# Kernel tuning notes

Hardware: AMD Instinct MI355X
Metric: run time of the kernel (lower is better)

The kernel has to match this reference:

```python
import jax, jax.numpy as jnp
import numpy as np

N_NODES = 50000
N_EDGES = 800000
N_GRAPHS = 500
IN_DIM, HID, OUT = 128, 64, 10


def setup_inputs() -> dict:
    key = jax.random.key(0)
    ks = jax.random.split(key, 12)
    x = jax.random.normal(ks[0], (N_NODES, IN_DIM), dtype=jnp.float32)
    edge_index = jax.random.randint(ks[1], (2, N_EDGES), 0, N_NODES, dtype=jnp.int32)
    batch = jnp.sort(jax.random.randint(ks[2], (N_NODES,), 0, N_GRAPHS, dtype=jnp.int32))
    def glorot(k, shape):
        lim = np.sqrt(6.0 / (shape[0] + shape[1]))
        return jax.random.uniform(k, shape, jnp.float32, -lim, lim)
    return {
        "x": x, "edge_index": edge_index, "batch": batch,
        "W1": glorot(ks[3], (IN_DIM, HID)), "b1": jnp.zeros((HID,), jnp.float32),
        "W2": glorot(ks[4], (HID, HID)),    "b2": jnp.zeros((HID,), jnp.float32),
        "W3": glorot(ks[5], (HID, HID)),    "b3": jnp.zeros((HID,), jnp.float32),
        "lin_W1": glorot(ks[6], (HID, HID)), "lin_b1": jnp.zeros((HID,), jnp.float32),
        "lin_W2": glorot(ks[7], (HID, OUT)), "lin_b2": jnp.zeros((OUT,), jnp.float32),
    }


def _gcn_conv(x, src, dst, deg_inv_sqrt, W, b):
    # PyG GCNConv: h = x @ W, then sym-normalized scatter-add over edges (self-loops included in src/dst)
    h = x @ W                                   # [N, out]
    norm = deg_inv_sqrt[src] * deg_inv_sqrt[dst]  # [E+N]
    msgs = h[src] * norm[:, None]               # [E+N, out]  (large gathered intermediate)
    out = jax.ops.segment_sum(msgs, dst, num_segments=N_NODES)
    return out + b


def reference(x, edge_index, batch, W1, b1, W2, b2, W3, b3, lin_W1, lin_b1, lin_W2, lin_b2):
    # add self-loops once; degree (with edge weight 1) computed on target nodes
    loops = jnp.arange(N_NODES, dtype=edge_index.dtype)
    src = jnp.concatenate([edge_index[0], loops])
    dst = jnp.concatenate([edge_index[1], loops])
    deg = jax.ops.segment_sum(jnp.ones_like(dst, dtype=x.dtype), dst, num_segments=N_NODES)
    deg_inv_sqrt = jnp.where(deg > 0, jax.lax.rsqrt(jnp.maximum(deg, 1e-12)), 0.0)

    h = jax.nn.relu(_gcn_conv(x, src, dst, deg_inv_sqrt, W1, b1))
    h = jax.nn.relu(_gcn_conv(h, src, dst, deg_inv_sqrt, W2, b2))
    h = jax.nn.relu(_gcn_conv(h, src, dst, deg_inv_sqrt, W3, b3))

    # global mean pool over graphs
    sums = jax.ops.segment_sum(h, batch, num_segments=N_GRAPHS)
    counts = jax.ops.segment_sum(jnp.ones((h.shape[0],), h.dtype), batch, num_segments=N_GRAPHS)
    pooled = sums / jnp.maximum(counts, 1.0)[:, None]  # [G, HID]

    # MLP head (dropout p=0 / eval -> identity)
    logits = jax.nn.relu(pooled @ lin_W1 + lin_b1) @ lin_W2 + lin_b2
    return (logits, jnp.zeros((), x.dtype))
```

## Files before the change

### kernel.cpp

```cpp
#include <hip/hip_runtime.h>
#include <hip/hip_bf16.h>

#define N_NODES 50000
#define N_EDGES 800000
#define N_GRAPHS 500
#define IN_DIM 128
#define HID 64
#define OUT_DIM 10
#define NB_BUCK ((N_NODES + 63) >> 6)
#define NBLK 256
#define BLDT 1024

__device__ __forceinline__ float bf2f(unsigned short u) {
    return __uint_as_float(((unsigned)u) << 16);
}
__device__ __forceinline__ unsigned short f2bf(float f) {
    unsigned x = __float_as_uint(f);
    x += 0x7fffu + ((x >> 16) & 1u);
    return (unsigned short)(x >> 16);
}
__device__ __forceinline__ void acc8(float a[8], uint4 r) {
    a[0] += __uint_as_float(r.x << 16);
    a[1] += __uint_as_float(r.x & 0xffff0000u);
    a[2] += __uint_as_float(r.y << 16);
    a[3] += __uint_as_float(r.y & 0xffff0000u);
    a[4] += __uint_as_float(r.z << 16);
    a[5] += __uint_as_float(r.z & 0xffff0000u);
    a[6] += __uint_as_float(r.w << 16);
    a[7] += __uint_as_float(r.w & 0xffff0000u);
}

__global__ __launch_bounds__(BLDT) void p1_hist_kernel(const int* __restrict__ dst,
                                                       int* __restrict__ bhist, int e, int epb) {
    __shared__ int h[NB_BUCK];
    int tid = threadIdx.x;
    int blk = blockIdx.x;
    for (int i = tid; i < NB_BUCK; i += BLDT) h[i] = 0;
    __syncthreads();
    int e0 = blk * epb;
    int e1 = e0 + epb;
    if (e1 > e) e1 = e;
    int i = e0 + tid * 4;
    for (; i + 3 < e1; i += BLDT * 4) {
        int4 d4 = *(const int4*)&dst[i];
        atomicAdd(&h[d4.x >> 6], 1);
        atomicAdd(&h[d4.y >> 6], 1);
        atomicAdd(&h[d4.z >> 6], 1);
        atomicAdd(&h[d4.w >> 6], 1);
    }
    for (int k = i; k < e1 && k < i + 4; ++k) atomicAdd(&h[dst[k] >> 6], 1);
    __syncthreads();
    for (int j = tid; j < NB_BUCK; j += BLDT) bhist[blk * NB_BUCK + j] = h[j];
}

__global__ __launch_bounds__(NBLK) void scanA_kernel(int* __restrict__ bhist,
                                                     int* __restrict__ bsum) {
    __shared__ int s[NBLK];
    int b = blockIdx.x;
    int t = threadIdx.x;
    int c = bhist[t * NB_BUCK + b];
    s[t] = c;
    __syncthreads();
    for (int off = 1; off < NBLK; off <<= 1) {
        int x = (t >= off) ? s[t - off] : 0;
        __syncthreads();
        s[t] += x;
        __syncthreads();
    }
    bhist[t * NB_BUCK + b] = s[t] - c;
    if (t == NBLK - 1) bsum[b] = s[t];
}

__global__ __launch_bounds__(BLDT) void p2_place_kernel(
    const int* __restrict__ src, const int* __restrict__ dst,
    const int* __restrict__ bsum, const int* __restrict__ base,
    unsigned* __restrict__ pairs, int* __restrict__ bstart, int e, int epb) {
    __shared__ int h[NB_BUCK];
    __shared__ int sb[NB_BUCK];
    __shared__ int ts[BLDT];
    int tid = threadIdx.x;
    int blk = blockIdx.x;
    int i0 = tid << 2;
    int v0 = 0, v1 = 0, v2 = 0, v3 = 0;
    if (i0 < NB_BUCK) v0 = bsum[i0];
    if (i0 + 1 < NB_BUCK) v1 = bsum[i0 + 1];
    if (i0 + 2 < NB_BUCK) v2 = bsum[i0 + 2];
    if (i0 + 3 < NB_BUCK) v3 = bsum[i0 + 3];
    int tsum = v0 + v1 + v2 + v3;
    ts[tid] = tsum;
    for (int i = tid; i < NB_BUCK; i += BLDT) h[i] = 0;
    __syncthreads();
    for (int off = 1; off < BLDT; off <<= 1) {
        int x = (tid >= off) ? ts[tid - off] : 0;
        __syncthreads();
        ts[tid] += x;
        __syncthreads();
    }
    int excl = ts[tid] - tsum;
    int s0 = excl;
    int s1 = s0 + v0;
    int s2 = s1 + v1;
    int s3 = s2 + v2;
    const int* bb = base + blk * NB_BUCK;
    if (i0 < NB_BUCK) sb[i0] = s0 + bb[i0];
    if (i0 + 1 < NB_BUCK) sb[i0 + 1] = s1 + bb[i0 + 1];
    if (i0 + 2 < NB_BUCK) sb[i0 + 2] = s2 + bb[i0 + 2];
    if (i0 + 3 < NB_BUCK) sb[i0 + 3] = s3 + bb[i0 + 3];
    if (blk == 0) {
        if (i0 < NB_BUCK) bstart[i0] = s0;
        if (i0 + 1 < NB_BUCK) bstart[i0 + 1] = s1;
        if (i0 + 2 < NB_BUCK) bstart[i0 + 2] = s2;
        if (i0 + 3 < NB_BUCK) bstart[i0 + 3] = s3;
        if (tid == 0) bstart[NB_BUCK] = e;
    }
    __syncthreads();
    int e0 = blk * epb;
    int e1 = e0 + epb;
    if (e1 > e) e1 = e;
    int i = e0 + tid * 4;
    for (; i + 3 < e1; i += BLDT * 4) {
        int4 d4 = *(const int4*)&dst[i];
        int4 s4 = *(const int4*)&src[i];
        int b0 = d4.x >> 6, b1 = d4.y >> 6, b2 = d4.z >> 6, b3 = d4.w >> 6;
        int r0 = atomicAdd(&h[b0], 1);
        int r1 = atomicAdd(&h[b1], 1);
        int r2 = atomicAdd(&h[b2], 1);
        int r3 = atomicAdd(&h[b3], 1);
        pairs[sb[b0] + r0] = ((unsigned)(d4.x & 63) << 16) | (unsigned)s4.x;
        pairs[sb[b1] + r1] = ((unsigned)(d4.y & 63) << 16) | (unsigned)s4.y;
        pairs[sb[b2] + r2] = ((unsigned)(d4.z & 63) << 16) | (unsigned)s4.z;
        pairs[sb[b3] + r3] = ((unsigned)(d4.w & 63) << 16) | (unsigned)s4.w;
    }
    for (int k = i; k < e1 && k < i + 4; ++k) {
        int d = dst[k];
        int b = d >> 6;
        int r = atomicAdd(&h[b], 1);
        pairs[sb[b] + r] = ((unsigned)(d & 63) << 16) | (unsigned)src[k];
    }
}

__global__ __launch_bounds__(256) void csr_lin1_kernel(
    const unsigned* __restrict__ pairs, const int* __restrict__ bstart,
    int* __restrict__ rs, float* __restrict__ dinv, int* __restrict__ csr_src,
    const float* __restrict__ A, const float* __restrict__ W,
    unsigned short* __restrict__ C, int n) {
    const int K = IN_DIM;
    __shared__ float As[64][K + 4];
    __shared__ float Ws[K][64];
    __shared__ int lcnt[64];
    __shared__ int lcur[64];
    __shared__ float sdinv[64];
    int b = blockIdx.x;
    int tid = threadIdx.x;
    int beg = bstart[b], end = bstart[b + 1];
    if (tid < 64) lcnt[tid] = 0;
    __syncthreads();
    for (int i = beg + tid; i < end; i += 256) atomicAdd(&lcnt[pairs[i] >> 16], 1);
    __syncthreads();
    if (tid < 64) {
        int c = lcnt[tid];
        int v = c;
#pragma unroll
        for (int off = 1; off < 64; off <<= 1) {
            int t = __shfl_up(v, off);
            if (tid >= off) v += t;
        }
        int excl = v - c;
        int node = b * 64 + tid;
        float dv = rsqrtf((float)(c + 1));
        if (node <= n) {
            rs[node] = beg + excl;
            if (node < n) dinv[node] = dv;
        }
        sdinv[tid] = dv;
        lcur[tid] = beg + excl;
    }
    __syncthreads();
    for (int i = beg + tid; i < end; i += 256) {
        unsigned p = pairs[i];
        int slot = atomicAdd(&lcur[p >> 16], 1);
        csr_src[slot] = (int)(p & 0xffffu);
    }

    int block0 = b * 64;
    int rows = n - block0;
    if (rows > 64) rows = 64;

    const float* Abase = A + (size_t)block0 * K;
    int totalA4 = (rows * K) >> 2;
    for (int i4 = tid; i4 < totalA4; i4 += 256) {
        int i = i4 << 2;
        float4 v = *(const float4*)(Abase + i);
        *(float4*)&As[i / K][i % K] = v;
    }
    {
        const float4* Wv = (const float4*)W;
        float4* Wsv = (float4*)&Ws[0][0];
        for (int i = tid; i < K * 16; i += 256) Wsv[i] = Wv[i];
    }
    __syncthreads();

    int tx = tid & 15;
    int ty = tid >> 4;
    float acc[4][4] = {};
#pragma unroll 2
    for (int k = 0; k < K; k += 4) {
        float4 a[4];
#pragma unroll
        for (int i = 0; i < 4; ++i) a[i] = *(const float4*)&As[ty * 4 + i][k];
        float4 w[4];
#pragma unroll
        for (int kk = 0; kk < 4; ++kk) w[kk] = *(const float4*)&Ws[k + kk][tx * 4];
#pragma unroll
        for (int i = 0; i < 4; ++i) {
            float av[4] = {a[i].x, a[i].y, a[i].z, a[i].w};
#pragma unroll
            for (int kk = 0; kk < 4; ++kk) {
                acc[i][0] += av[kk] * w[kk].x;
                acc[i][1] += av[kk] * w[kk].y;
                acc[i][2] += av[kk] * w[kk].z;
                acc[i][3] += av[kk] * w[kk].w;
            }
        }
    }

#pragma unroll
    for (int i = 0; i < 4; ++i) {
        int r = ty * 4 + i;
        if (r < rows) {
            float s = sdinv[r];
            ushort4 v;
            v.x = f2bf(acc[i][0] * s);
            v.y = f2bf(acc[i][1] * s);
            v.z = f2bf(acc[i][2] * s);
            v.w = f2bf(acc[i][3] * s);
            *(ushort4*)&C[(size_t)(block0 + r) * 64 + tx * 4] = v;
        }
    }
}

__global__ __launch_bounds__(256) void gather_lin_kernel(
    const unsigned short* __restrict__ hs, const int* __restrict__ rs,
    const int* __restrict__ csr_src, const float* __restrict__ dinv,
    const float* __restrict__ bias, const float* __restrict__ W,
    unsigned short* __restrict__ C, int n) {
    const int K = HID;
    __shared__ float As[64][K + 4];
    __shared__ float Ws[K][64];
    int tid = threadIdx.x;
    int b = blockIdx.x;
    int block0 = b * 64;
    int rows = n - block0;
    if (rows > 64) rows = 64;

    {
        const float4* Wv = (const float4*)W;
        float4* Wsv = (float4*)&Ws[0][0];
        for (int i = tid; i < K * 16; i += 256) Wsv[i] = Wv[i];
    }

    int grp = tid >> 3;
    int lg = tid & 7;
    int f8 = lg << 3;
    float4 bb0 = *(const float4*)&bias[f8];
    float4 bb1 = *(const float4*)&bias[f8 + 4];

    for (int r = grp; r < 64; r += 32) {
        int node = block0 + r;
        float a[8] = {0.f, 0.f, 0.f, 0.f, 0.f, 0.f, 0.f, 0.f};
        if (node < n) {
            int beg = rs[node], end = rs[node + 1];
            {
                uint4 u = *(const uint4*)&hs[(size_t)node * 64 + f8];
                acc8(a, u);
            }
            int j = beg;
            for (; j + 3 < end; j += 4) {
                int s0 = csr_src[j];
                int s1 = csr_src[j + 1];
                int s2 = csr_src[j + 2];
                int s3 = csr_src[j + 3];
                uint4 r0 = *(const uint4*)&hs[(size_t)s0 * 64 + f8];
                uint4 r1 = *(const uint4*)&hs[(size_t)s1 * 64 + f8];
                uint4 r2 = *(const uint4*)&hs[(size_t)s2 * 64 + f8];
                uint4 r3 = *(const uint4*)&hs[(size_t)s3 * 64 + f8];
                acc8(a, r0);
                acc8(a, r1);
                acc8(a, r2);
                acc8(a, r3);
            }
            if (j + 1 < end) {
                int s0 = csr_src[j];
                int s1 = csr_src[j + 1];
                uint4 r0 = *(const uint4*)&hs[(size_t)s0 * 64 + f8];
                uint4 r1 = *(const uint4*)&hs[(size_t)s1 * 64 + f8];
                acc8(a, r0);
                acc8(a, r1);
                j += 2;
            }
            if (j < end) {
                int s0 = csr_src[j];
                uint4 r0 = *(const uint4*)&hs[(size_t)s0 * 64 + f8];
                acc8(a, r0);
            }
            float sc = dinv[node];
            a[0] = fmaxf(a[0] * sc + bb0.x, 0.f);
            a[1] = fmaxf(a[1] * sc + bb0.y, 0.f);
            a[2] = fmaxf(a[2] * sc + bb0.z, 0.f);
            a[3] = fmaxf(a[3] * sc + bb0.w, 0.f);
            a[4] = fmaxf(a[4] * sc + bb1.x, 0.f);
            a[5] = fmaxf(a[5] * sc + bb1.y, 0.f);
            a[6] = fmaxf(a[6] * sc + bb1.z, 0.f);
            a[7] = fmaxf(a[7] * sc + bb1.w, 0.f);
        }
        float4 w0 = {a[0], a[1], a[2], a[3]};
        float4 w1 = {a[4], a[5], a[6], a[7]};
        *(float4*)&As[r][f8] = w0;
        *(float4*)&As[r][f8 + 4] = w1;
    }
    __syncthreads();

    int tx = tid & 15;
    int ty = tid >> 4;
    float acc[4][4] = {};
#pragma unroll 2
    for (int k = 0; k < K; k += 4) {
        float4 a[4];
#pragma unroll
        for (int i = 0; i < 4; ++i) a[i] = *(const float4*)&As[ty * 4 + i][k];
        float4 w[4];
#pragma unroll
        for (int kk = 0; kk < 4; ++kk) w[kk] = *(const float4*)&Ws[k + kk][tx * 4];
#pragma unroll
        for (int i = 0; i < 4; ++i) {
            float av[4] = {a[i].x, a[i].y, a[i].z, a[i].w};
#pragma unroll
            for (int kk = 0; kk < 4; ++kk) {
                acc[i][0] += av[kk] * w[kk].x;
                acc[i][1] += av[kk] * w[kk].y;
                acc[i][2] += av[kk] * w[kk].z;
                acc[i][3] += av[kk] * w[kk].w;
            }
        }
    }

#pragma unroll
    for (int i = 0; i < 4; ++i) {
        int r = ty * 4 + i;
        if (r < rows) {
            float s = dinv[block0 + r];
            ushort4 v;
            v.x = f2bf(acc[i][0] * s);
            v.y = f2bf(acc[i][1] * s);
            v.z = f2bf(acc[i][2] * s);
            v.w = f2bf(acc[i][3] * s);
            *(ushort4*)&C[(size_t)(block0 + r) * 64 + tx * 4] = v;
        }
    }
}

__global__ __launch_bounds__(256) void gather_kernel(
    const unsigned short* __restrict__ hs, const int* __restrict__ rs,
    const int* __restrict__ csr_src, const float* __restrict__ dinv,
    const float* __restrict__ bias, unsigned short* __restrict__ outp, int n) {
    int wave = threadIdx.x >> 6;
    int node = blockIdx.x * 4 + wave;
    if (node >= n) return;
    int lane = threadIdx.x & 63;
    int eg = lane >> 3;
    int f8 = (lane & 7) << 3;
    int beg = rs[node], end = rs[node + 1];
    int len = end - beg;
    int q = (len + 7) >> 3;
    int mb = beg + eg * q;
    int me = mb + q;
    if (me > end) me = end;
    float a[8] = {0.f, 0.f, 0.f, 0.f, 0.f, 0.f, 0.f, 0.f};
    if (eg == 0) {
        uint4 r = *(const uint4*)&hs[(size_t)node * 64 + f8];
        acc8(a, r);
    }
    int j = mb;
    for (; j + 3 < me; j += 4) {
        int s0 = csr_src[j];
        int s1 = csr_src[j + 1];
        int s2 = csr_src[j + 2];
        int s3 = csr_src[j + 3];
        uint4 r0 = *(const uint4*)&hs[(size_t)s0 * 64 + f8];
        uint4 r1 = *(const uint4*)&hs[(size_t)s1 * 64 + f8];
        uint4 r2 = *(const uint4*)&hs[(size_t)s2 * 64 + f8];
        uint4 r3 = *(const uint4*)&hs[(size_t)s3 * 64 + f8];
        acc8(a, r0);
        acc8(a, r1);
        acc8(a, r2);
        acc8(a, r3);
    }
    if (j + 1 < me) {
        int s0 = csr_src[j];
        int s1 = csr_src[j + 1];
        uint4 r0 = *(const uint4*)&hs[(size_t)s0 * 64 + f8];
        uint4 r1 = *(const uint4*)&hs[(size_t)s1 * 64 + f8];
        acc8(a, r0);
        acc8(a, r1);
        j += 2;
    }
    if (j < me) {
        int s0 = csr_src[j];
        uint4 r0 = *(const uint4*)&hs[(size_t)s0 * 64 + f8];
        acc8(a, r0);
    }
#pragma unroll
    for (int k = 0; k < 8; ++k) a[k] += __shfl_xor(a[k], 8);
#pragma unroll
    for (int k = 0; k < 8; ++k) a[k] += __shfl_xor(a[k], 16);
#pragma unroll
    for (int k = 0; k < 8; ++k) a[k] += __shfl_xor(a[k], 32);
    if (eg == 0) {
        float s = dinv[node];
        float4 b0 = *(const float4*)&bias[f8];
        float4 b1 = *(const float4*)&bias[f8 + 4];
        float v0 = fmaxf(a[0] * s + b0.x, 0.f);
        float v1 = fmaxf(a[1] * s + b0.y, 0.f);
        float v2 = fmaxf(a[2] * s + b0.z, 0.f);
        float v3 = fmaxf(a[3] * s + b0.w, 0.f);
        float v4 = fmaxf(a[4] * s + b1.x, 0.f);
        float v5 = fmaxf(a[5] * s + b1.y, 0.f);
        float v6 = fmaxf(a[6] * s + b1.z, 0.f);
        float v7 = fmaxf(a[7] * s + b1.w, 0.f);
        uint4 o;
        o.x = (unsigned)f2bf(v0) | ((unsigned)f2bf(v1) << 16);
        o.y = (unsigned)f2bf(v2) | ((unsigned)f2bf(v3) << 16);
        o.z = (unsigned)f2bf(v4) | ((unsigned)f2bf(v5) << 16);
        o.w = (unsigned)f2bf(v6) | ((unsigned)f2bf(v7) << 16);
        *(uint4*)&outp[(size_t)node * 64 + f8] = o;
    }
}

__device__ __forceinline__ int lower_bound_dev(const int* __restrict__ a, int n, int v) {
    int lo = 0, hi = n;
    while (lo < hi) {
        int m = (lo + hi) >> 1;
        if (a[m] < v) lo = m + 1; else hi = m;
    }
    return lo;
}

__global__ __launch_bounds__(1024) void pool_head_kernel(
    const unsigned short* __restrict__ h, const int* __restrict__ batch,
    const float* __restrict__ W1, const float* __restrict__ b1,
    const float* __restrict__ W2, const float* __restrict__ b2,
    float* __restrict__ out, int nNodes, int nGraphs) {
    __shared__ float psum[16][64];
    __shared__ float p[64];
    __shared__ float t64[64];
    int g = blockIdx.x;
    int tid = threadIdx.x;
    int f = tid & 63;
    int q = tid >> 6;
    int lo = lower_bound_dev(batch, nNodes, g);
    int hi = lower_bound_dev(batch, nNodes, g + 1);
    float sum = 0.0f;
    for (int i = lo + q; i < hi; i += 16) sum += bf2f(h[(size_t)i * 64 + f]);
    psum[q][f] = sum;
    __syncthreads();
    if (tid < 64) {
        float s = 0.0f;
#pragma unroll
        for (int w = 0; w < 16; ++w) s += psum[w][f];
        float inv = 1.0f / fmaxf((float)(hi - lo), 1.0f);
        p[f] = s * inv;
        float acc = b1[f];
#pragma unroll
        for (int k = 0; k < 64; ++k) acc += p[k] * W1[k * 64 + f];
        t64[f] = fmaxf(acc, 0.0f);
        if (f < OUT_DIM) {
            float acc2 = b2[f];
#pragma unroll
            for (int k = 0; k < 64; ++k) acc2 += t64[k] * W2[k * OUT_DIM + f];
            out[g * OUT_DIM + f] = acc2;
        }
        if (g == 0 && f == 0) out[nGraphs * OUT_DIM] = 0.0f;
    }
}

extern "C" void kernel_launch(void* const* d_in, const int* in_sizes, int n_in,
                              void* d_out, int out_size, void* d_ws, size_t ws_size,
                              hipStream_t stream) {
    const float* x      = (const float*)d_in[0];
    const int*   eidx   = (const int*)d_in[1];
    const int*   batch  = (const int*)d_in[2];
    const float* W1     = (const float*)d_in[3];
    const float* b1     = (const float*)d_in[4];
    const float* W2     = (const float*)d_in[5];
    const float* b2     = (const float*)d_in[6];
    const float* W3     = (const float*)d_in[7];
    const float* b3     = (const float*)d_in[8];
    const float* lin_W1 = (const float*)d_in[9];
    const float* lin_b1 = (const float*)d_in[10];
    const float* lin_W2 = (const float*)d_in[11];
    const float* lin_b2 = (const float*)d_in[12];
    float* out = (float*)d_out;

    const int E = in_sizes[1] / 2;
    const int N = N_NODES;
    const int NF = N * HID;
    int epb = (E + NBLK - 1) / NBLK;
    epb = (epb + 7) & ~7;

    const int* src = eidx;
    const int* dst = eidx + E;

    unsigned short* buf1 = (unsigned short*)d_ws;
    unsigned short* buf2 = buf1 + NF;
    float* dinv = (float*)(buf2 + NF);
    int* bhist  = (int*)(dinv + N);
    int* bsum   = bhist + NBLK * NB_BUCK;
    int* bstart = bsum + NB_BUCK;
    int* rs     = bstart + NB_BUCK + 1;
    int* csr_src = rs + N + 1;
    unsigned* pairs = (unsigned*)(csr_src + E);

    const int TILES = (N + 63) / 64;
    const int GBLK = (N + 3) / 4;

    p1_hist_kernel<<<NBLK, BLDT, 0, stream>>>(dst, bhist, E, epb);
    scanA_kernel<<<NB_BUCK, NBLK, 0, stream>>>(bhist, bsum);
    p2_place_kernel<<<NBLK, BLDT, 0, stream>>>(src, dst, bsum, bhist, pairs, bstart, E, epb);

    csr_lin1_kernel<<<TILES, 256, 0, stream>>>(pairs, bstart, rs, dinv, csr_src,
                                               x, W1, buf1, N);

    gather_lin_kernel<<<TILES, 256, 0, stream>>>(buf1, rs, csr_src, dinv, b1, W2, buf2, N);

    gather_lin_kernel<<<TILES, 256, 0, stream>>>(buf2, rs, csr_src, dinv, b2, W3, buf1, N);

    gather_kernel<<<GBLK, 256, 0, stream>>>(buf1, rs, csr_src, dinv, b3, buf2, N);

    pool_head_kernel<<<N_GRAPHS, 1024, 0, stream>>>(buf2, batch, lin_W1, lin_b1, lin_W2, lin_b2,
                                                    out, N, N_GRAPHS);
}
```

Measured before the change: 219.2 us.

## Fuse final gather with mean-pool via atomics, shrink gather tiles to 32 rows

The last aggregation layer now accumulates per-graph sums directly with run-length atomics into a global buffer, which is zeroed inside the histogram kernel. This removes the bf16 write and reread of the final node features and the separate pooling pass. The head kernel becomes a small 64-thread kernel that reads those sums. Gather-linear kernels now use 32-row tiles, doubling block count for more parallelism, and the neighbour loop is unrolled by 8 for more loads in flight. Float atomics make the sum order nondeterministic, and the smaller tiles load the weight matrix into shared memory twice as often.

```diff
diff --git a/kernel.cpp b/kernel.cpp
--- a/kernel.cpp
+++ b/kernel.cpp
@@ -30,11 +30,72 @@
     a[7] += __uint_as_float(r.w & 0xffff0000u);
 }
 
+__device__ __forceinline__ void gather_node(const unsigned short* __restrict__ hs,
+                                            const int* __restrict__ csr_src,
+                                            int node, int beg, int end, int f8, float a[8]) {
+    {
+        uint4 u = *(const uint4*)&hs[(size_t)node * 64 + f8];
+        acc8(a, u);
+    }
+    int j = beg;
+    for (; j + 7 < end; j += 8) {
+        int s0 = csr_src[j];
+        int s1 = csr_src[j + 1];
+        int s2 = csr_src[j + 2];
+        int s3 = csr_src[j + 3];
+        int s4 = csr_src[j + 4];
+        int s5 = csr_src[j + 5];
+        int s6 = csr_src[j + 6];
+        int s7 = csr_src[j + 7];
+        uint4 r0 = *(const uint4*)&hs[(size_t)s0 * 64 + f8];
+        uint4 r1 = *(const uint4*)&hs[(size_t)s1 * 64 + f8];
+        uint4 r2 = *(const uint4*)&hs[(size_t)s2 * 64 + f8];
+        uint4 r3 = *(const uint4*)&hs[(size_t)s3 * 64 + f8];
+        uint4 r4 = *(const uint4*)&hs[(size_t)s4 * 64 + f8];
+        uint4 r5 = *(const uint4*)&hs[(size_t)s5 * 64 + f8];
+        uint4 r6 = *(const uint4*)&hs[(size_t)s6 * 64 + f8];
+        uint4 r7 = *(const uint4*)&hs[(size_t)s7 * 64 + f8];
+        acc8(a, r0); acc8(a, r1); acc8(a, r2); acc8(a, r3);
+        acc8(a, r4); acc8(a, r5); acc8(a, r6); acc8(a, r7);
+    }
+    if (j + 3 < end) {
+        int s0 = csr_src[j];
+        int s1 = csr_src[j + 1];
+        int s2 = csr_src[j + 2];
+        int s3 = csr_src[j + 3];
+        uint4 r0 = *(const uint4*)&hs[(size_t)s0 * 64 + f8];
+        uint4 r1 = *(const uint4*)&hs[(size_t)s1 * 64 + f8];
+        uint4 r2 = *(const uint4*)&hs[(size_t)s2 * 64 + f8];
+        uint4 r3 = *(const uint4*)&hs[(size_t)s3 * 64 + f8];
+        acc8(a, r0); acc8(a, r1); acc8(a, r2); acc8(a, r3);
+        j += 4;
+    }
+    if (j + 1 < end) {
+        int s0 = csr_src[j];
+        int s1 = csr_src[j + 1];
+        uint4 r0 = *(const uint4*)&hs[(size_t)s0 * 64 + f8];
+        uint4 r1 = *(const uint4*)&hs[(size_t)s1 * 64 + f8];
+        acc8(a, r0); acc8(a, r1);
+        j += 2;
+    }
+    if (j < end) {
+        int s0 = csr_src[j];
+        uint4 r0 = *(const uint4*)&hs[(size_t)s0 * 64 + f8];
+        acc8(a, r0);
+    }
+}
+
 __global__ __launch_bounds__(BLDT) void p1_hist_kernel(const int* __restrict__ dst,
-                                                       int* __restrict__ bhist, int e, int epb) {
+                                                       int* __restrict__ bhist,
+                                                       float* __restrict__ gsum,
+                                                       int e, int epb) {
     __shared__ int h[NB_BUCK];
     int tid = threadIdx.x;
     int blk = blockIdx.x;
+    {
+        int z = blk * BLDT + tid;
+        if (z < N_GRAPHS * HID) gsum[z] = 0.0f;
+    }
     for (int i = tid; i < NB_BUCK; i += BLDT) h[i] = 0;
     __syncthreads();
     int e0 = blk * epb;
@@ -245,13 +306,12 @@
     const float* __restrict__ bias, const float* __restrict__ W,
     unsigned short* __restrict__ C, int n) {
     const int K = HID;
-    __shared__ float As[64][K + 4];
+    __shared__ float As[32][K + 4];
     __shared__ float Ws[K][64];
     int tid = threadIdx.x;
-    int b = blockIdx.x;
-    int block0 = b * 64;
+    int block0 = blockIdx.x * 32;
     int rows = n - block0;
-    if (rows > 64) rows = 64;
+    if (rows > 32) rows = 32;
 
     {
         const float4* Wv = (const float4*)W;
@@ -265,75 +325,43 @@
     float4 bb0 = *(const float4*)&bias[f8];
     float4 bb1 = *(const float4*)&bias[f8 + 4];
 
-    for (int r = grp; r < 64; r += 32) {
-        int node = block0 + r;
-        float a[8] = {0.f, 0.f, 0.f, 0.f, 0.f, 0.f, 0.f, 0.f};
-        if (node < n) {
-            int beg = rs[node], end = rs[node + 1];
-            {
-                uint4 u = *(const uint4*)&hs[(size_t)node * 64 + f8];
-                acc8(a, u);
-            }
-            int j = beg;
-            for (; j + 3 < end; j += 4) {
-                int s0 = csr_src[j];
-                int s1 = csr_src[j + 1];
-                int s2 = csr_src[j + 2];
-                int s3 = csr_src[j + 3];
-                uint4 r0 = *(const uint4*)&hs[(size_t)s0 * 64 + f8];
-                uint4 r1 = *(const uint4*)&hs[(size_t)s1 * 64 + f8];
-                uint4 r2 = *(const uint4*)&hs[(size_t)s2 * 64 + f8];
-                uint4 r3 = *(const uint4*)&hs[(size_t)s3 * 64 + f8];
-                acc8(a, r0);
-                acc8(a, r1);
-                acc8(a, r2);
-                acc8(a, r3);
-            }
-            if (j + 1 < end) {
-                int s0 = csr_src[j];
-                int s1 = csr_src[j + 1];
-                uint4 r0 = *(const uint4*)&hs[(size_t)s0 * 64 + f8];
-                uint4 r1 = *(const uint4*)&hs[(size_t)s1 * 64 + f8];
-                acc8(a, r0);
-                acc8(a, r1);
-                j += 2;
-            }
-            if (j < end) {
-                int s0 = csr_src[j];
-                uint4 r0 = *(const uint4*)&hs[(size_t)s0 * 64 + f8];
-                acc8(a, r0);
-            }
-            float sc = dinv[node];
-            a[0] = fmaxf(a[0] * sc + bb0.x, 0.f);
-            a[1] = fmaxf(a[1] * sc + bb0.y, 0.f);
-            a[2] = fmaxf(a[2] * sc + bb0.z, 0.f);
-            a[3] = fmaxf(a[3] * sc + bb0.w, 0.f);
-            a[4] = fmaxf(a[4] * sc + bb1.x, 0.f);
-            a[5] = fmaxf(a[5] * sc + bb1.y, 0.f);
-            a[6] = fmaxf(a[6] * sc + bb1.z, 0.f);
-            a[7] = fmaxf(a[7] * sc + bb1.w, 0.f);
-        }
+    int node = block0 + grp;
+    float a[8] = {0.f, 0.f, 0.f, 0.f, 0.f, 0.f, 0.f, 0.f};
+    if (node < n) {
+        int beg = rs[node], end = rs[node + 1];
+        gather_node(hs, csr_src, node, beg, end, f8, a);
+        float sc = dinv[node];
+        a[0] = fmaxf(a[0] * sc + bb0.x, 0.f);
+        a[1] = fmaxf(a[1] * sc + bb0.y, 0.f);
+        a[2] = fmaxf(a[2] * sc + bb0.z, 0.f);
+        a[3] = fmaxf(a[3] * sc + bb0.w, 0.f);
+        a[4] = fmaxf(a[4] * sc + bb1.x, 0.f);
+        a[5] = fmaxf(a[5] * sc + bb1.y, 0.f);
+        a[6] = fmaxf(a[6] * sc + bb1.z, 0.f);
+        a[7] = fmaxf(a[7] * sc + bb1.w, 0.f);
+    }
+    {
         float4 w0 = {a[0], a[1], a[2], a[3]};
         float4 w1 = {a[4], a[5], a[6], a[7]};
-        *(float4*)&As[r][f8] = w0;
-        *(float4*)&As[r][f8 + 4] = w1;
+        *(float4*)&As[grp][f8] = w0;
+        *(float4*)&As[grp][f8 + 4] = w1;
     }
     __syncthreads();
 
     int tx = tid & 15;
     int ty = tid >> 4;
-    float acc[4][4] = {};
+    float acc[2][4] = {};
 #pragma unroll 2
     for (int k = 0; k < K; k += 4) {
-        float4 a[4];
-#pragma unroll
-        for (int i = 0; i < 4; ++i) a[i] = *(const float4*)&As[ty * 4 + i][k];
+        float4 aa[2];
+#pragma unroll
+        for (int i = 0; i < 2; ++i) aa[i] = *(const float4*)&As[ty * 2 + i][k];
         float4 w[4];
 #pragma unroll
         for (int kk = 0; kk < 4; ++kk) w[kk] = *(const float4*)&Ws[k + kk][tx * 4];
 #pragma unroll
-        for (int i = 0; i < 4; ++i) {
-            float av[4] = {a[i].x, a[i].y, a[i].z, a[i].w};
+        for (int i = 0; i < 2; ++i) {
+            float av[4] = {aa[i].x, aa[i].y, aa[i].z, aa[i].w};
 #pragma unroll
             for (int kk = 0; kk < 4; ++kk) {
                 acc[i][0] += av[kk] * w[kk].x;
@@ -345,8 +373,8 @@
     }
 
 #pragma unroll
-    for (int i = 0; i < 4; ++i) {
-        int r = ty * 4 + i;
+    for (int i = 0; i < 2; ++i) {
+        int r = ty * 2 + i;
         if (r < rows) {
             float s = dinv[block0 + r];
             ushort4 v;
@@ -359,80 +387,64 @@
     }
 }
 
-__global__ __launch_bounds__(256) void gather_kernel(
+__global__ __launch_bounds__(256) void gather_pool_kernel(
     const unsigned short* __restrict__ hs, const int* __restrict__ rs,
     const int* __restrict__ csr_src, const float* __restrict__ dinv,
-    const float* __restrict__ bias, unsigned short* __restrict__ outp, int n) {
-    int wave = threadIdx.x >> 6;
-    int node = blockIdx.x * 4 + wave;
-    if (node >= n) return;
-    int lane = threadIdx.x & 63;
-    int eg = lane >> 3;
-    int f8 = (lane & 7) << 3;
-    int beg = rs[node], end = rs[node + 1];
-    int len = end - beg;
-    int q = (len + 7) >> 3;
-    int mb = beg + eg * q;
-    int me = mb + q;
-    if (me > end) me = end;
+    const float* __restrict__ bias, const int* __restrict__ batch,
+    float* __restrict__ gsum, int n) {
+    __shared__ float As[32][68];
+    int tid = threadIdx.x;
+    int block0 = blockIdx.x * 32;
+    int rows = n - block0;
+    if (rows > 32) rows = 32;
+
+    int grp = tid >> 3;
+    int lg = tid & 7;
+    int f8 = lg << 3;
+    float4 bb0 = *(const float4*)&bias[f8];
+    float4 bb1 = *(const float4*)&bias[f8 + 4];
+
+    int node = block0 + grp;
     float a[8] = {0.f, 0.f, 0.f, 0.f, 0.f, 0.f, 0.f, 0.f};
-    if (eg == 0) {
-        uint4 r = *(const uint4*)&hs[(size_t)node * 64 + f8];
-        acc8(a, r);
-    }
-    int j = mb;
-    for (; j + 3 < me; j += 4) {
-        int s0 = csr_src[j];
-        int s1 = csr_src[j + 1];
-        int s2 = csr_src[j + 2];
-        int s3 = csr_src[j + 3];
-        uint4 r0 = *(const uint4*)&hs[(size_t)s0 * 64 + f8];
-        uint4 r1 = *(const uint4*)&hs[(size_t)s1 * 64 + f8];
-        uint4 r2 = *(const uint4*)&hs[(size_t)s2 * 64 + f8];
-        uint4 r3 = *(const uint4*)&hs[(size_t)s3 * 64 + f8];
-        acc8(a, r0);
-        acc8(a, r1);
-        acc8(a, r2);
-        acc8(a, r3);
-    }
-    if (j + 1 < me) {
-        int s0 = csr_src[j];
-        int s1 = csr_src[j + 1];
-        uint4 r0 = *(const uint4*)&hs[(size_t)s0 * 64 + f8];
-        uint4 r1 = *(const uint4*)&hs[(size_t)s1 * 64 + f8];
-        acc8(a, r0);
-        acc8(a, r1);
-        j += 2;
-    }
-    if (j < me) {
-        int s0 = csr_src[j];
-        uint4 r0 = *(const uint4*)&hs[(size_t)s0 * 64 + f8];
-        acc8(a, r0);
-    }
-#pragma unroll
-    for (int k = 0; k < 8; ++k) a[k] += __shfl_xor(a[k], 8);
-#pragma unroll
-    for (int k = 0; k < 8; ++k) a[k] += __shfl_xor(a[k], 16);
-#pragma unroll
-    for (int k = 0; k < 8; ++k) a[k] += __shfl_xor(a[k], 32);
-    if (eg == 0) {
-        float s = dinv[node];
-        float4 b0 = *(const float4*)&bias[f8];
-        float4 b1 = *(const float4*)&bias[f8 + 4];
-        float v0 = fmaxf(a[0] * s + b0.x, 0.f);
-        float v1 = fmaxf(a[1] * s + b0.y, 0.f);
-        float v2 = fmaxf(a[2] * s + b0.z, 0.f);
-        float v3 = fmaxf(a[3] * s + b0.w, 0.f);
-        float v4 = fmaxf(a[4] * s + b1.x, 0.f);
-        float v5 = fmaxf(a[5] * s + b1.y, 0.f);
-        float v6 = fmaxf(a[6] * s + b1.z, 0.f);
-        float v7 = fmaxf(a[7] * s + b1.w, 0.f);
-        uint4 o;
-        o.x = (unsigned)f2bf(v0) | ((unsigned)f2bf(v1) << 16);
-        o.y = (unsigned)f2bf(v2) | ((unsigned)f2bf(v3) << 16);
-        o.z = (unsigned)f2bf(v4) | ((unsigned)f2bf(v5) << 16);
-        o.w = (unsigned)f2bf(v6) | ((unsigned)f2bf(v7) << 16);
-        *(uint4*)&outp[(size_t)node * 64 + f8] = o;
+    if (node < n) {
+        int beg = rs[node], end = rs[node + 1];
+        gather_node(hs, csr_src, node, beg, end, f8, a);
+        float sc = dinv[node];
+        a[0] = fmaxf(a[0] * sc + bb0.x, 0.f);
+        a[1] = fmaxf(a[1] * sc + bb0.y, 0.f);
+        a[2] = fmaxf(a[2] * sc + bb0.z, 0.f);
+        a[3] = fmaxf(a[3] * sc + bb0.w, 0.f);
+        a[4] = fmaxf(a[4] * sc + bb1.x, 0.f);
+        a[5] = fmaxf(a[5] * sc + bb1.y, 0.f);
+        a[6] = fmaxf(a[6] * sc + bb1.z, 0.f);
+        a[7] = fmaxf(a[7] * sc + bb1.w, 0.f);
+    }
+    {
+        float4 w0 = {a[0], a[1], a[2], a[3]};
+        float4 w1 = {a[4], a[5], a[6], a[7]};
+        *(float4*)&As[grp][f8] = w0;
+        *(float4*)&As[grp][f8 + 4] = w1;
+    }
+    __syncthreads();
+
+    int q = tid >> 6;
+    int f = tid & 63;
+    int r0 = q * 8;
+    int r1 = r0 + 8;
+    if (r1 > rows) r1 = rows;
+    if (r0 < rows) {
+        int gprev = batch[block0 + r0];
+        float run = 0.0f;
+        for (int r = r0; r < r1; ++r) {
+            int g = batch[block0 + r];
+            if (g != gprev) {
+                atomicAdd(&gsum[(size_t)gprev * 64 + f], run);
+                run = 0.0f;
+                gprev = g;
+            }
+            run += As[r][f];
+        }
+        atomicAdd(&gsum[(size_t)gprev * 64 + f], run);
     }
 }
 
@@ -445,42 +457,32 @@
     return lo;
 }
 
-__global__ __launch_bounds__(1024) void pool_head_kernel(
-    const unsigned short* __restrict__ h, const int* __restrict__ batch,
+__global__ __launch_bounds__(64) void head_kernel(
+    const float* __restrict__ gsum, const int* __restrict__ batch,
     const float* __restrict__ W1, const float* __restrict__ b1,
     const float* __restrict__ W2, const float* __restrict__ b2,
     float* __restrict__ out, int nNodes, int nGraphs) {
-    __shared__ float psum[16][64];
     __shared__ float p[64];
     __shared__ float t64[64];
     int g = blockIdx.x;
-    int tid = threadIdx.x;
-    int f = tid & 63;
-    int q = tid >> 6;
+    int f = threadIdx.x;
     int lo = lower_bound_dev(batch, nNodes, g);
     int hi = lower_bound_dev(batch, nNodes, g + 1);
-    float sum = 0.0f;
-    for (int i = lo + q; i < hi; i += 16) sum += bf2f(h[(size_t)i * 64 + f]);
-    psum[q][f] = sum;
-    __syncthreads();
-    if (tid < 64) {
-        float s = 0.0f;
-#pragma unroll
-        for (int w = 0; w < 16; ++w) s += psum[w][f];
-        float inv = 1.0f / fmaxf((float)(hi - lo), 1.0f);
-        p[f] = s * inv;
-        float acc = b1[f];
-#pragma unroll
-        for (int k = 0; k < 64; ++k) acc += p[k] * W1[k * 64 + f];
-        t64[f] = fmaxf(acc, 0.0f);
-        if (f < OUT_DIM) {
-            float acc2 = b2[f];
-#pragma unroll
-            for (int k = 0; k < 64; ++k) acc2 += t64[k] * W2[k * OUT_DIM + f];
-            out[g * OUT_DIM + f] = acc2;
-        }
-        if (g == 0 && f == 0) out[nGraphs * OUT_DIM] = 0.0f;
-    }
+    float inv = 1.0f / fmaxf((float)(hi - lo), 1.0f);
+    p[f] = gsum[(size_t)g * 64 + f] * inv;
+    __syncthreads();
+    float acc = b1[f];
+#pragma unroll
+    for (int k = 0; k < 64; ++k) acc += p[k] * W1[k * 64 + f];
+    t64[f] = fmaxf(acc, 0.0f);
+    __syncthreads();
+    if (f < OUT_DIM) {
+        float acc2 = b2[f];
+#pragma unroll
+        for (int k = 0; k < 64; ++k) acc2 += t64[k] * W2[k * OUT_DIM + f];
+        out[g * OUT_DIM + f] = acc2;
+    }
+    if (g == 0 && f == 0) out[nGraphs * OUT_DIM] = 0.0f;
 }
 
 extern "C" void kernel_launch(void* const* d_in, const int* in_sizes, int n_in,
@@ -519,23 +521,24 @@
     int* rs     = bstart + NB_BUCK + 1;
     int* csr_src = rs + N + 1;
     unsigned* pairs = (unsigned*)(csr_src + E);
+    float* gsum = (float*)(pairs + E);
 
     const int TILES = (N + 63) / 64;
-    const int GBLK = (N + 3) / 4;
-
-    p1_hist_kernel<<<NBLK, BLDT, 0, stream>>>(dst, bhist, E, epb);
+    const int G32 = (N + 31) / 32;
+
+    p1_hist_kernel<<<NBLK, BLDT, 0, stream>>>(dst, bhist, gsum, E, epb);
     scanA_kernel<<<NB_BUCK, NBLK, 0, stream>>>(bhist, bsum);
     p2_place_kernel<<<NBLK, BLDT, 0, stream>>>(src, dst, bsum, bhist, pairs, bstart, E, epb);
 
     csr_lin1_kernel<<<TILES, 256, 0, stream>>>(pairs, bstart, rs, dinv, csr_src,
                                                x, W1, buf1, N);
 
-    gather_lin_kernel<<<TILES, 256, 0, stream>>>(buf1, rs, csr_src, dinv, b1, W2, buf2, N);
-
-    gather_lin_kernel<<<TILES, 256, 0, stream>>>(buf2, rs, csr_src, dinv, b2, W3, buf1, N);
-
-    gather_kernel<<<GBLK, 256, 0, stream>>>(buf1, rs, csr_src, dinv, b3, buf2, N);
-
-    pool_head_kernel<<<N_GRAPHS, 1024, 0, stream>>>(buf2, batch, lin_W1, lin_b1, lin_W2, lin_b2,
-                                                    out, N, N_GRAPHS);
-}
+    gather_lin_kernel<<<G32, 256, 0, stream>>>(buf1, rs, csr_src, dinv, b1, W2, buf2, N);
+
+    gather_lin_kernel<<<G32, 256, 0, stream>>>(buf2, rs, csr_src, dinv, b2, W3, buf1, N);
+
+    gather_pool_kernel<<<G32, 256, 0, stream>>>(buf1, rs, csr_src, dinv, b3, batch, gsum, N);
+
+    head_kernel<<<N_GRAPHS, 64, 0, stream>>>(gsum, batch, lin_W1, lin_b1, lin_W2, lin_b2,
+                                             out, N, N_GRAPHS);
+}
```

Result: faster. 205.5 us (-6.3%).
